# Performance work log

Measured on AMD Instinct MI355X. Metric: run time of the kernel, lower is better.

Reference implementation:

```python
import jax, jax.numpy as jnp
import numpy as np

LN_EPS = 1e-5


def _layer_norm(x, scale, bias):
    mu = jnp.mean(x, axis=-1, keepdims=True)
    var = jnp.mean(jnp.square(x - mu), axis=-1, keepdims=True)
    return (x - mu) * jax.lax.rsqrt(var + LN_EPS) * scale + bias


def setup_inputs() -> dict:
    key = jax.random.key(0)
    B, N, C_Z, C_H = 1, 512, 128, 128
    ks = jax.random.split(key, 8)
    s = 1.0 / np.sqrt(C_Z)
    inp = {
        "z": jax.random.normal(ks[0], (B, N, N, C_Z), dtype=jnp.float32),
        "mask": jnp.ones((B, N, N), dtype=jnp.float32),
        # gated / plain projections from c_z -> c_hidden
        "w_a_p": jax.random.normal(ks[1], (C_Z, C_H), dtype=jnp.float32) * s,
        "b_a_p": jnp.zeros((C_H,), dtype=jnp.float32),
        "w_a_g": jnp.zeros((C_Z, C_H), dtype=jnp.float32),  # gating init: zeros, bias ones
        "b_a_g": jnp.ones((C_H,), dtype=jnp.float32),
        "w_b_p": jax.random.normal(ks[2], (C_Z, C_H), dtype=jnp.float32) * s,
        "b_b_p": jnp.zeros((C_H,), dtype=jnp.float32),
        "w_b_g": jnp.zeros((C_Z, C_H), dtype=jnp.float32),
        "b_b_g": jnp.ones((C_H,), dtype=jnp.float32),
        # output gate c_z -> c_z (gating init)
        "w_g": jnp.zeros((C_Z, C_Z), dtype=jnp.float32),
        "b_g": jnp.ones((C_Z,), dtype=jnp.float32),
        # final projection c_hidden -> c_z ('final' init: zeros; use small randn for a nontrivial test)
        "w_z": jax.random.normal(ks[3], (C_H, C_Z), dtype=jnp.float32) * (1.0 / np.sqrt(C_H)),
        "b_z": jnp.zeros((C_Z,), dtype=jnp.float32),
        "ln_in_scale": jnp.ones((C_Z,), dtype=jnp.float32),
        "ln_in_bias": jnp.zeros((C_Z,), dtype=jnp.float32),
        "ln_out_scale": jnp.ones((C_H,), dtype=jnp.float32),
        "ln_out_bias": jnp.zeros((C_H,), dtype=jnp.float32),
    }
    return inp


def reference(z, mask, w_a_p, b_a_p, w_a_g, b_a_g, w_b_p, b_b_p, w_b_g, b_b_g,
              w_g, b_g, w_z, b_z, ln_in_scale, ln_in_bias, ln_out_scale, ln_out_bias):
    # tmu_type == 'outgoing'
    z = _layer_norm(z, ln_in_scale, ln_in_bias)          # [B,N,N,Cz]
    m = mask[..., None]                                   # [B,N,N,1]
    a = jax.nn.sigmoid(z @ w_a_g + b_a_g) * m * (z @ w_a_p + b_a_p)  # [B,N,N,Ch]
    b = jax.nn.sigmoid(z @ w_b_g + b_b_g) * m * (z @ w_b_p + b_b_p)  # [B,N,N,Ch]
    # outgoing: p[b,i,j,c] = sum_k a[b,i,k,c] * b[b,j,k,c]
    x = jnp.einsum("bikc,bjkc->bijc", a, b)              # [B,N,N,Ch]
    x = _layer_norm(x, ln_out_scale, ln_out_bias)
    x = x @ w_z + b_z                                    # [B,N,N,Cz]
    g = jax.nn.sigmoid(z @ w_g + b_g)                    # [B,N,N,Cz]
    return x * g
```

## Files before the change

kernel.cpp:

```cpp
#include <hip/hip_runtime.h>

typedef __attribute__((ext_vector_type(8))) short short8;
typedef __attribute__((ext_vector_type(4))) short short4v;
typedef __attribute__((ext_vector_type(4))) float float4v;

#define NDIM 512
#define NN (NDIM*NDIM)
#define CD 128

__device__ __forceinline__ unsigned short f2b(float f) {
  union { float f; unsigned u; } v; v.f = f;
  unsigned r = v.u + 0x7FFFu + ((v.u >> 16) & 1u);
  return (unsigned short)(r >> 16);
}
__device__ __forceinline__ float b2f(unsigned short h) {
  union { unsigned u; float f; } v; v.u = ((unsigned)h) << 16; return v.f;
}
__device__ __forceinline__ float sigmoidf_(float x) { return 1.f / (1.f + __expf(-x)); }
__device__ __forceinline__ unsigned pk2(float a, float b) {
  unsigned r;
  asm("v_cvt_pk_bf16_f32 %0, %1, %2" : "=v"(r) : "v"(a), "v"(b));
  return r;
}
__device__ __forceinline__ float4v mfma16(short8 a, short8 b, float4v c) {
  return __builtin_amdgcn_mfma_f32_16x16x32_bf16(a, b, c, 0, 0, 0);
}
__device__ __forceinline__ void gl_lds16(const short* g, short* l) {
  __builtin_amdgcn_global_load_lds(
      (const __attribute__((address_space(1))) unsigned int*)g,
      (__attribute__((address_space(3))) unsigned int*)l, 16, 0, 0);
}

__device__ __forceinline__ short8 fragr(const short* buf, int row, int j) {
  return *(const short8*)(buf + row * 128 + ((j ^ (row & 15)) << 3));
}
__device__ __forceinline__ void stg_w(short* buf, int row, int ku, unsigned v) {
  *(unsigned*)&buf[row * 128 + ((((ku >> 2) ^ (row & 15)) << 3) + ((ku & 3) << 1))] = v;
}

__global__ __launch_bounds__(256) void kPrepW(
    const float* __restrict__ w0, const float* __restrict__ w1,
    const float* __restrict__ w2, const float* __restrict__ w3,
    const float* __restrict__ w4, short* __restrict__ wt)
{
  const int wi = blockIdx.y;
  const float* W = wi==0 ? w0 : wi==1 ? w1 : wi==2 ? w2 : wi==3 ? w3 : w4;
  const int e = blockIdx.x * 256 + threadIdx.x;
  const int k = e >> 7, n = e & 127;
  wt[wi * 16384 + n * 128 + k] = (short)f2b(W[k * CD + n]);
}

__global__ __launch_bounds__(1024, 4) void kProj(
    const float* __restrict__ z, const float* __restrict__ mask,
    const short* __restrict__ wT,
    const float* __restrict__ b_a_p, const float* __restrict__ b_a_g,
    const float* __restrict__ b_b_p, const float* __restrict__ b_b_g,
    const float* __restrict__ b_g,
    const float* __restrict__ ln_s, const float* __restrict__ ln_b,
    short* __restrict__ a_t, short* __restrict__ b_t, short* __restrict__ g_out)
{
  __shared__ short zln[128 * 128];
  __shared__ short sS[128 * 128];
  __shared__ short wA[128 * 128];
  __shared__ short wB[128 * 128];
  const int t = threadIdx.x;
  const int r0 = blockIdx.x * 128;
  const int w = t >> 6, l = t & 63, lr = l & 15, lg = l >> 4;
  const int wr = (w >> 1) * 16;
  const int hc = (w & 1) * 64;

#define STAGE2(BUF, SLOT) do { _Pragma("unroll") for (int i_=0;i_<2;++i_) {  \
    int U_ = i_*1024 + t; int row_ = U_ >> 4, u_ = U_ & 15;                  \
    gl_lds16(wT + (SLOT)*16384 + row_*128 + ((u_^(row_&15))<<3), (BUF)+U_*8); } } while(0)

  STAGE2(wA, 1);
  STAGE2(wB, 0);

  {
    const int row = t >> 3, q = t & 7;
    const float* zp = z + (size_t)(r0 + row) * CD + q * 16;
    float x[16];
#pragma unroll
    for (int i = 0; i < 4; ++i) {
      float4v v = *(const float4v*)(zp + i * 4);
#pragma unroll
      for (int e = 0; e < 4; ++e) x[i*4+e] = v[e];
    }
    float s = 0.f;
#pragma unroll
    for (int i = 0; i < 16; ++i) s += x[i];
    s += __shfl_xor(s, 1, 64);
    s += __shfl_xor(s, 2, 64);
    s += __shfl_xor(s, 4, 64);
    const float mu = s * (1.f/128.f);
    float vs = 0.f;
#pragma unroll
    for (int i = 0; i < 16; ++i) { float d = x[i]-mu; vs += d*d; }
    vs += __shfl_xor(vs, 1, 64);
    vs += __shfl_xor(vs, 2, 64);
    vs += __shfl_xor(vs, 4, 64);
    const float rstd = rsqrtf(vs * (1.f/128.f) + 1e-5f);
#pragma unroll
    for (int i = 0; i < 16; i += 2) {
      int c = q*16 + i;
      float y0 = (x[i]  -mu)*rstd*ln_s[c]   + ln_b[c];
      float y1 = (x[i+1]-mu)*rstd*ln_s[c+1] + ln_b[c+1];
      int addr = row*128 + (((c>>3) ^ (row & 15)) << 3) + (c & 7);
      *(unsigned*)(&zln[addr]) = pk2(y0, y1);
    }
  }

  float bga[4], bpa[4], bgb[4], bpb[4];
#pragma unroll
  for (int cf = 0; cf < 4; ++cf) {
    int ci = hc + cf*16 + lr;
    bga[cf] = b_a_g[ci]; bpa[cf] = b_a_p[ci];
    bgb[cf] = b_b_g[ci]; bpb[cf] = b_b_p[ci];
  }
  float mrow[4];
#pragma unroll
  for (int jj = 0; jj < 4; ++jj) mrow[jj] = mask[r0 + wr + lg*4 + jj];

  __syncthreads();

  short8 af[4];
#pragma unroll
  for (int ks = 0; ks < 4; ++ks)
    af[ks] = fragr(zln, wr + lr, ks*4 + lg);

  float4v accG[4], accB[4];
  float sg[4][4];

#define ZERO4(A) do { _Pragma("unroll") for (int c_=0;c_<4;++c_) A[c_] = (float4v){0.f,0.f,0.f,0.f}; } while(0)

#define WP(ACC, BUF) do { ZERO4(ACC);                                      \
  _Pragma("unroll") for (int ks_=0; ks_<4; ++ks_)                          \
    _Pragma("unroll") for (int cf_=0; cf_<4; ++cf_) {                      \
      short8 wf_ = fragr(BUF, hc + cf_*16 + lr, ks_*4 + lg);               \
      ACC[cf_] = mfma16(af[ks_], wf_, ACC[cf_]);                           \
    } } while(0)

#define SIG4(BG) do { _Pragma("unroll") for (int cf_=0;cf_<4;++cf_)        \
    _Pragma("unroll") for (int j_=0;j_<4;++j_)                             \
      sg[cf_][j_] = sigmoidf_(accG[cf_][j_] + BG[cf_]) * mrow[j_]; } while(0)

#define PKAB(BP) do { _Pragma("unroll") for (int cf_=0;cf_<4;++cf_) {      \
    float v0_ = sg[cf_][0]*(accB[cf_][0]+BP[cf_]);                         \
    float v1_ = sg[cf_][1]*(accB[cf_][1]+BP[cf_]);                         \
    float v2_ = sg[cf_][2]*(accB[cf_][2]+BP[cf_]);                         \
    float v3_ = sg[cf_][3]*(accB[cf_][3]+BP[cf_]);                         \
    int ch_ = hc + cf_*16 + lr, ku_ = (wr >> 1) + lg*2;                    \
    stg_w(sS, ch_, ku_,   pk2(v0_, v1_));                                  \
    stg_w(sS, ch_, ku_+1, pk2(v2_, v3_)); } } while(0)

#define STORE64A(DST) do { int ch_ = t >> 3;                               \
  _Pragma("unroll") for (int i_=0;i_<2;++i_) {                             \
    int cL_ = (t & 7)*2 + i_;                                              \
    *(short8*)(DST + (size_t)ch_*NN + r0 + cL_*8) = fragr(sS, ch_, cL_);   \
  } } while(0)

  WP(accG, wA);
  WP(accB, wB);
  SIG4(bga);
  PKAB(bpa);
  __syncthreads();

  STAGE2(wA, 3);
  STAGE2(wB, 2);
  STORE64A(a_t);
  __syncthreads();

  WP(accG, wA);
  WP(accB, wB);
  SIG4(bgb);
  PKAB(bpb);
  __syncthreads();

  STAGE2(wA, 4);
  STORE64A(b_t);
  __syncthreads();

  {
    float4v accG2[4];
    ZERO4(accG2);
#pragma unroll
    for (int ks = 0; ks < 4; ++ks)
#pragma unroll
      for (int cf = 0; cf < 4; ++cf) {
        short8 wf = fragr(wA, hc + cf*16 + lr, ks*4 + lg);
        accG2[cf] = mfma16(wf, af[ks], accG2[cf]);
      }
#pragma unroll
    for (int cf = 0; cf < 4; ++cf) {
      float4v bgv = *(const float4v*)(b_g + hc + cf*16 + lg*4);
      float v0 = sigmoidf_(accG2[cf][0] + bgv[0]);
      float v1 = sigmoidf_(accG2[cf][1] + bgv[1]);
      float v2 = sigmoidf_(accG2[cf][2] + bgv[2]);
      float v3 = sigmoidf_(accG2[cf][3] + bgv[3]);
      int row = wr + lr, ku = (hc >> 1) + cf*8 + lg*2;
      stg_w(sS, row, ku,   pk2(v0, v1));
      stg_w(sS, row, ku+1, pk2(v2, v3));
    }
  }
  __syncthreads();

  {
    int row = t >> 3;
#pragma unroll
    for (int i = 0; i < 2; ++i) {
      int cL = (t & 7)*2 + i;
      *(short8*)(g_out + (size_t)(r0 + row)*CD + cL*8) = fragr(sS, row, cL);
    }
  }
}

__global__ __launch_bounds__(256, 2) void kEinsum(const short* __restrict__ a_t,
                                                  const short* __restrict__ b_t,
                                                  short* __restrict__ x_t)
{
  __shared__ short As[2][128 * 64];
  __shared__ short Bs[2][128 * 64];
  const int t = threadIdx.x;
  const int d = blockIdx.x;
  const int c = (d & 7) * 16 + (d >> 7);
  const int tile = (d >> 3) & 15;
  const int i0 = (tile >> 2) * 128;
  const int j0 = (tile & 3) * 128;
  const size_t abase = (size_t)c * NN;
  const int w = t >> 6, l = t & 63, lr = l & 15, lg = l >> 4;
  const int wr = w >> 1, wc = w & 1;

  const short* gA[4]; const short* gB[4]; int ldsU[4];
#pragma unroll
  for (int q = 0; q < 4; ++q) {
    int U = q * 256 + t;
    int row = U >> 3, u = U & 7;
    int swz = ((u ^ (row & 7)) << 3);
    gA[q] = a_t + abase + (size_t)(i0 + row) * NDIM + swz;
    gB[q] = b_t + abase + (size_t)(j0 + row) * NDIM + swz;
    ldsU[q] = U * 8;
  }

#define STAGE_E(buf, k0) do { _Pragma("unroll") for (int q_=0;q_<4;++q_) { \
    gl_lds16(gA[q_] + (k0), &As[buf][ldsU[q_]]);                           \
    gl_lds16(gB[q_] + (k0), &Bs[buf][ldsU[q_]]); } } while(0)

  float4v acc[4][4];
#pragma unroll
  for (int m = 0; m < 4; ++m)
#pragma unroll
    for (int n = 0; n < 4; ++n) acc[m][n] = (float4v){0.f,0.f,0.f,0.f};

  STAGE_E(0, 0);
  __syncthreads();
  int cur = 0;
#pragma unroll
  for (int it = 0; it < 8; ++it) {
    if (it < 7) STAGE_E(cur ^ 1, (it + 1) * 64);
    short8 afr[4][2], bfr[4][2];
#pragma unroll
    for (int m = 0; m < 4; ++m)
#pragma unroll
      for (int ks = 0; ks < 2; ++ks) {
        int row = wr*64 + m*16 + lr, j = ks*4 + lg;
        afr[m][ks] = *(const short8*)(&As[cur][row*64 + ((j ^ (row & 7)) << 3)]);
      }
#pragma unroll
    for (int n = 0; n < 4; ++n)
#pragma unroll
      for (int ks = 0; ks < 2; ++ks) {
        int row = wc*64 + n*16 + lr, j = ks*4 + lg;
        bfr[n][ks] = *(const short8*)(&Bs[cur][row*64 + ((j ^ (row & 7)) << 3)]);
      }
    __builtin_amdgcn_s_setprio(1);
#pragma unroll
    for (int ks = 0; ks < 2; ++ks)
#pragma unroll
      for (int m = 0; m < 4; ++m)
#pragma unroll
        for (int n = 0; n < 4; ++n)
          acc[m][n] = mfma16(bfr[n][ks], afr[m][ks], acc[m][n]);
    __builtin_amdgcn_s_setprio(0);
    __syncthreads();
    cur ^= 1;
  }
  short* Xs = &As[0][0];
#pragma unroll
  for (int m = 0; m < 4; ++m)
#pragma unroll
    for (int n = 0; n < 4; ++n) {
      int il = wr*64 + m*16 + lr;
      int ku = wc*32 + n*8 + lg*2;
      stg_w(Xs, il, ku,   pk2(acc[m][n][0], acc[m][n][1]));
      stg_w(Xs, il, ku+1, pk2(acc[m][n][2], acc[m][n][3]));
    }
  __syncthreads();
#pragma unroll
  for (int i = 0; i < 8; ++i) {
    int il = t >> 1, cL = (t & 1)*8 + i;
    *(short8*)(x_t + abase + (size_t)(i0 + il)*NDIM + j0 + cL*8) = fragr(Xs, il, cL);
  }
}

__global__ __launch_bounds__(256, 2) void kOut(
    const short* __restrict__ x_t, const short* __restrict__ g_in,
    const float* __restrict__ w_z, const float* __restrict__ b_z,
    const float* __restrict__ ln_s, const float* __restrict__ ln_b,
    float* __restrict__ out)
{
  __shared__ short xs[128 * 72];
  __shared__ short xln[64 * 128];
  __shared__ short sW[128 * 128];
  const int t = threadIdx.x;
  const int r0 = blockIdx.x * 64;
  const int w = t >> 6, l = t & 63, lr = l & 15, lg = l >> 4;

#pragma unroll
  for (int i = 0; i < 8; ++i) {
    int flat = i * 256 + t;
    int kp = flat >> 5, k = kp * 2, n4 = (flat & 31) * 4;
    float4v va = *(const float4v*)(w_z + (size_t)k * CD + n4);
    float4v vb = *(const float4v*)(w_z + (size_t)(k + 1) * CD + n4);
#pragma unroll
    for (int j = 0; j < 4; ++j) {
      int row = n4 + j;
      int addr = row * 128 + (((k >> 3) ^ (row & 15)) << 3) + (k & 7);
      *(unsigned*)(&sW[addr]) = pk2(va[j], vb[j]);
    }
  }
#pragma unroll
  for (int it = 0; it < 4; ++it) {
    int v = it * 256 + t; int cc = v >> 3; int u = v & 7;
    int up = u ^ ((cc >> 3) & 7);
    *(short8*)&xs[cc * 72 + up * 8] = *(const short8*)(x_t + (size_t)cc * NN + r0 + u * 8);
  }
  __syncthreads();
  {
    const int r = t >> 2, q = t & 3;
    float x[32];
#pragma unroll
    for (int i = 0; i < 32; ++i) {
      int c = q * 32 + i;
      x[i] = b2f((unsigned short)xs[c * 72 + (((r >> 3) ^ ((c >> 3) & 7)) << 3) + (r & 7)]);
    }
    float s = 0.f;
#pragma unroll
    for (int i = 0; i < 32; ++i) s += x[i];
    s += __shfl_xor(s, 1, 64);
    s += __shfl_xor(s, 2, 64);
    const float mu = s * (1.f/128.f);
    float vs = 0.f;
#pragma unroll
    for (int i = 0; i < 32; ++i) { float d = x[i]-mu; vs += d*d; }
    vs += __shfl_xor(vs, 1, 64);
    vs += __shfl_xor(vs, 2, 64);
    const float rstd = rsqrtf(vs * (1.f/128.f) + 1e-5f);
#pragma unroll
    for (int i = 0; i < 32; ++i) {
      int c = q*32 + i;
      float y = (x[i]-mu)*rstd*ln_s[c] + ln_b[c];
      xln[r*128 + (((c>>3) ^ (r & 15)) << 3) + (c & 7)] = (short)f2b(y);
    }
  }
  __syncthreads();
  short8 af[4];
#pragma unroll
  for (int ks = 0; ks < 4; ++ks)
    af[ks] = fragr(xln, w*16 + lr, ks*4 + lg);

  float4v acc[8];
#pragma unroll
  for (int cf = 0; cf < 8; ++cf) acc[cf] = (float4v){0.f,0.f,0.f,0.f};
#pragma unroll
  for (int ks = 0; ks < 4; ++ks)
#pragma unroll
    for (int cf = 0; cf < 8; ++cf) {
      short8 wf = fragr(sW, cf*16 + lr, ks*4 + lg);
      acc[cf] = mfma16(wf, af[ks], acc[cf]);
    }
  __syncthreads();
  float* fWs = (float*)sW;
  const int orow = r0 + w*16 + lr;
  const int rl = w*16 + lr;
#pragma unroll
  for (int cf = 0; cf < 8; ++cf) {
    float4v bzv = *(const float4v*)(b_z + cf*16 + lg*4);
    short4v gv = *(const short4v*)(g_in + (size_t)orow * CD + cf*16 + lg*4);
    float4v o;
#pragma unroll
    for (int j = 0; j < 4; ++j)
      o[j] = (acc[cf][j] + bzv[j]) * b2f((unsigned short)gv[j]);
    *(float4v*)&fWs[rl*128 + (((cf*4+lg) ^ (rl & 15)) << 2)] = o;
  }
  __syncthreads();
#pragma unroll
  for (int i = 0; i < 8; ++i) {
    int row = t >> 2, cL = (t & 3)*8 + i;
    *(float4v*)(out + (size_t)(r0 + row)*CD + cL*4) =
        *(const float4v*)&fWs[row*128 + ((cL ^ (row & 15)) << 2)];
  }
}

extern "C" void kernel_launch(void* const* d_in, const int* in_sizes, int n_in,
                              void* d_out, int out_size, void* d_ws, size_t ws_size,
                              hipStream_t stream) {
  (void)in_sizes; (void)n_in; (void)out_size; (void)ws_size;
  const float* z     = (const float*)d_in[0];
  const float* mask  = (const float*)d_in[1];
  const float* w_a_p = (const float*)d_in[2];
  const float* b_a_p = (const float*)d_in[3];
  const float* w_a_g = (const float*)d_in[4];
  const float* b_a_g = (const float*)d_in[5];
  const float* w_b_p = (const float*)d_in[6];
  const float* b_b_p = (const float*)d_in[7];
  const float* w_b_g = (const float*)d_in[8];
  const float* b_b_g = (const float*)d_in[9];
  const float* w_g   = (const float*)d_in[10];
  const float* b_g   = (const float*)d_in[11];
  const float* w_z   = (const float*)d_in[12];
  const float* b_z   = (const float*)d_in[13];
  const float* ln_i_s = (const float*)d_in[14];
  const float* ln_i_b = (const float*)d_in[15];
  const float* ln_o_s = (const float*)d_in[16];
  const float* ln_o_b = (const float*)d_in[17];

  short* a_t = (short*)d_ws;
  short* b_t = a_t + (size_t)CD*NN;
  short* g_s = b_t + (size_t)CD*NN;
  short* x_t = g_s + (size_t)CD*NN;
  short* wT  = x_t;

  hipLaunchKernelGGL(kPrepW, dim3(64, 5), dim3(256), 0, stream,
                     w_a_p, w_a_g, w_b_p, w_b_g, w_g, wT);
  hipLaunchKernelGGL(kProj, dim3(NN/128), dim3(1024), 0, stream,
                     z, mask, wT, b_a_p, b_a_g, b_b_p, b_b_g, b_g,
                     ln_i_s, ln_i_b, a_t, b_t, g_s);
  hipLaunchKernelGGL(kEinsum, dim3(2048), dim3(256), 0, stream, a_t, b_t, x_t);
  hipLaunchKernelGGL(kOut, dim3(NN/64), dim3(256), 0, stream,
                     x_t, g_s, w_z, b_z, ln_o_s, ln_o_b, (float*)d_out);
}
```

Baseline: 347.3 us.

## Restructure projection kernel to register-resident weights and pipelined 32-row tiles

The projection kernel moves from 1024-thread blocks that stage all weights into LDS to 256-thread blocks. Each block handles one half of the hidden channels for 128 rows and keeps its weight fragments in registers. It walks four 32-row sub-tiles with double-buffered LayerNorm output and prefetches the next sub-tile's z into registers, so global loads overlap with MFMA work. The aim is lower LDS use, higher occupancy and latency hiding, at the cost of recomputing LayerNorm twice (once per channel half) and higher register pressure from the 20 held weight fragments.

Result: slower. 359.9 us (+3.6%).

```diff
diff --git a/kernel.cpp b/kernel.cpp
--- a/kernel.cpp
+++ b/kernel.cpp
@@ -36,6 +36,18 @@
 }
 __device__ __forceinline__ void stg_w(short* buf, int row, int ku, unsigned v) {
   *(unsigned*)&buf[row * 128 + ((((ku >> 2) ^ (row & 15)) << 3) + ((ku & 3) << 1))] = v;
+}
+__device__ __forceinline__ short8 frag32(const short* buf, int ch, int j) {
+  return *(const short8*)(buf + ch * 32 + ((j ^ (ch & 3)) << 3));
+}
+__device__ __forceinline__ void stg32(short* buf, int ch, int ku, unsigned v) {
+  *(unsigned*)&buf[ch * 32 + ((((ku >> 2) ^ (ch & 3)) << 3) + ((ku & 3) << 1))] = v;
+}
+__device__ __forceinline__ short8 frag64(const short* buf, int row, int j) {
+  return *(const short8*)(buf + row * 64 + ((j ^ (row & 7)) << 3));
+}
+__device__ __forceinline__ void stg64(short* buf, int row, int ku, unsigned v) {
+  *(unsigned*)&buf[row * 64 + ((((ku >> 2) ^ (row & 7)) << 3) + ((ku & 3) << 1))] = v;
 }
 
 __global__ __launch_bounds__(256) void kPrepW(
@@ -50,7 +62,7 @@
   wt[wi * 16384 + n * 128 + k] = (short)f2b(W[k * CD + n]);
 }
 
-__global__ __launch_bounds__(1024, 4) void kProj(
+__global__ __launch_bounds__(256, 2) void kProj(
     const float* __restrict__ z, const float* __restrict__ mask,
     const short* __restrict__ wT,
     const float* __restrict__ b_a_p, const float* __restrict__ b_a_g,
@@ -59,159 +71,135 @@
     const float* __restrict__ ln_s, const float* __restrict__ ln_b,
     short* __restrict__ a_t, short* __restrict__ b_t, short* __restrict__ g_out)
 {
-  __shared__ short zln[128 * 128];
-  __shared__ short sS[128 * 128];
-  __shared__ short wA[128 * 128];
-  __shared__ short wB[128 * 128];
-  const int t = threadIdx.x;
-  const int r0 = blockIdx.x * 128;
-  const int w = t >> 6, l = t & 63, lr = l & 15, lg = l >> 4;
-  const int wr = (w >> 1) * 16;
-  const int hc = (w & 1) * 64;
-
-#define STAGE2(BUF, SLOT) do { _Pragma("unroll") for (int i_=0;i_<2;++i_) {  \
-    int U_ = i_*1024 + t; int row_ = U_ >> 4, u_ = U_ & 15;                  \
-    gl_lds16(wT + (SLOT)*16384 + row_*128 + ((u_^(row_&15))<<3), (BUF)+U_*8); } } while(0)
-
-  STAGE2(wA, 1);
-  STAGE2(wB, 0);
-
-  {
-    const int row = t >> 3, q = t & 7;
-    const float* zp = z + (size_t)(r0 + row) * CD + q * 16;
-    float x[16];
-#pragma unroll
-    for (int i = 0; i < 4; ++i) {
-      float4v v = *(const float4v*)(zp + i * 4);
-#pragma unroll
-      for (int e = 0; e < 4; ++e) x[i*4+e] = v[e];
-    }
-    float s = 0.f;
-#pragma unroll
-    for (int i = 0; i < 16; ++i) s += x[i];
-    s += __shfl_xor(s, 1, 64);
-    s += __shfl_xor(s, 2, 64);
-    s += __shfl_xor(s, 4, 64);
-    const float mu = s * (1.f/128.f);
-    float vs = 0.f;
-#pragma unroll
-    for (int i = 0; i < 16; ++i) { float d = x[i]-mu; vs += d*d; }
-    vs += __shfl_xor(vs, 1, 64);
-    vs += __shfl_xor(vs, 2, 64);
-    vs += __shfl_xor(vs, 4, 64);
-    const float rstd = rsqrtf(vs * (1.f/128.f) + 1e-5f);
-#pragma unroll
-    for (int i = 0; i < 16; i += 2) {
-      int c = q*16 + i;
-      float y0 = (x[i]  -mu)*rstd*ln_s[c]   + ln_b[c];
-      float y1 = (x[i+1]-mu)*rstd*ln_s[c+1] + ln_b[c+1];
-      int addr = row*128 + (((c>>3) ^ (row & 15)) << 3) + (c & 7);
-      *(unsigned*)(&zln[addr]) = pk2(y0, y1);
-    }
-  }
-
-  float bga[4], bpa[4], bgb[4], bpb[4];
-#pragma unroll
-  for (int cf = 0; cf < 4; ++cf) {
-    int ci = hc + cf*16 + lr;
-    bga[cf] = b_a_g[ci]; bpa[cf] = b_a_p[ci];
-    bgb[cf] = b_b_g[ci]; bpb[cf] = b_b_p[ci];
-  }
-  float mrow[4];
-#pragma unroll
-  for (int jj = 0; jj < 4; ++jj) mrow[jj] = mask[r0 + wr + lg*4 + jj];
-
-  __syncthreads();
-
-  short8 af[4];
-#pragma unroll
-  for (int ks = 0; ks < 4; ++ks)
-    af[ks] = fragr(zln, wr + lr, ks*4 + lg);
-
-  float4v accG[4], accB[4];
-  float sg[4][4];
-
-#define ZERO4(A) do { _Pragma("unroll") for (int c_=0;c_<4;++c_) A[c_] = (float4v){0.f,0.f,0.f,0.f}; } while(0)
-
-#define WP(ACC, BUF) do { ZERO4(ACC);                                      \
-  _Pragma("unroll") for (int ks_=0; ks_<4; ++ks_)                          \
-    _Pragma("unroll") for (int cf_=0; cf_<4; ++cf_) {                      \
-      short8 wf_ = fragr(BUF, hc + cf_*16 + lr, ks_*4 + lg);               \
-      ACC[cf_] = mfma16(af[ks_], wf_, ACC[cf_]);                           \
-    } } while(0)
-
-#define SIG4(BG) do { _Pragma("unroll") for (int cf_=0;cf_<4;++cf_)        \
-    _Pragma("unroll") for (int j_=0;j_<4;++j_)                             \
-      sg[cf_][j_] = sigmoidf_(accG[cf_][j_] + BG[cf_]) * mrow[j_]; } while(0)
-
-#define PKAB(BP) do { _Pragma("unroll") for (int cf_=0;cf_<4;++cf_) {      \
-    float v0_ = sg[cf_][0]*(accB[cf_][0]+BP[cf_]);                         \
-    float v1_ = sg[cf_][1]*(accB[cf_][1]+BP[cf_]);                         \
-    float v2_ = sg[cf_][2]*(accB[cf_][2]+BP[cf_]);                         \
-    float v3_ = sg[cf_][3]*(accB[cf_][3]+BP[cf_]);                         \
-    int ch_ = hc + cf_*16 + lr, ku_ = (wr >> 1) + lg*2;                    \
-    stg_w(sS, ch_, ku_,   pk2(v0_, v1_));                                  \
-    stg_w(sS, ch_, ku_+1, pk2(v2_, v3_)); } } while(0)
-
-#define STORE64A(DST) do { int ch_ = t >> 3;                               \
-  _Pragma("unroll") for (int i_=0;i_<2;++i_) {                             \
-    int cL_ = (t & 7)*2 + i_;                                              \
-    *(short8*)(DST + (size_t)ch_*NN + r0 + cL_*8) = fragr(sS, ch_, cL_);   \
-  } } while(0)
-
-  WP(accG, wA);
-  WP(accB, wB);
-  SIG4(bga);
-  PKAB(bpa);
-  __syncthreads();
-
-  STAGE2(wA, 3);
-  STAGE2(wB, 2);
-  STORE64A(a_t);
-  __syncthreads();
-
-  WP(accG, wA);
-  WP(accB, wB);
-  SIG4(bgb);
-  PKAB(bpb);
-  __syncthreads();
-
-  STAGE2(wA, 4);
-  STORE64A(b_t);
-  __syncthreads();
-
-  {
-    float4v accG2[4];
-    ZERO4(accG2);
+  __shared__ short zln[2][32 * 128];
+  __shared__ short sSa[64 * 32];
+  __shared__ short sSb[64 * 32];
+  __shared__ short sSg[32 * 64];
+
+  const int tid = threadIdx.x;
+  const int bid = blockIdx.x;
+  const int sw = (bid & 7) * 512 + (bid >> 3);
+  const int ch_half = sw & 1;
+  const int tg = sw >> 1;
+  const int r0 = tg * 128;
+  const int w = tid >> 6, l = tid & 63, lr = l & 15, lg = l >> 4;
+  const int chw = ch_half * 64 + w * 16;
+  const int lrow = tid >> 3, q = tid & 7;
+
+  short8 wfr[5][4];
+#pragma unroll
+  for (int s = 0; s < 5; ++s)
 #pragma unroll
     for (int ks = 0; ks < 4; ++ks)
-#pragma unroll
-      for (int cf = 0; cf < 4; ++cf) {
-        short8 wf = fragr(wA, hc + cf*16 + lr, ks*4 + lg);
-        accG2[cf] = mfma16(wf, af[ks], accG2[cf]);
-      }
-#pragma unroll
-    for (int cf = 0; cf < 4; ++cf) {
-      float4v bgv = *(const float4v*)(b_g + hc + cf*16 + lg*4);
-      float v0 = sigmoidf_(accG2[cf][0] + bgv[0]);
-      float v1 = sigmoidf_(accG2[cf][1] + bgv[1]);
-      float v2 = sigmoidf_(accG2[cf][2] + bgv[2]);
-      float v3 = sigmoidf_(accG2[cf][3] + bgv[3]);
-      int row = wr + lr, ku = (hc >> 1) + cf*8 + lg*2;
-      stg_w(sS, row, ku,   pk2(v0, v1));
-      stg_w(sS, row, ku+1, pk2(v2, v3));
-    }
-  }
-  __syncthreads();
-
-  {
-    int row = t >> 3;
-#pragma unroll
-    for (int i = 0; i < 2; ++i) {
-      int cL = (t & 7)*2 + i;
-      *(short8*)(g_out + (size_t)(r0 + row)*CD + cL*8) = fragr(sS, row, cL);
-    }
-  }
+      wfr[s][ks] = *(const short8*)(wT + s*16384 + (chw + lr)*128 + ks*32 + lg*8);
+
+  const float bga = b_a_g[chw + lr], bpa = b_a_p[chw + lr];
+  const float bgb = b_b_g[chw + lr], bpb = b_b_p[chw + lr];
+  const float4v bgv = *(const float4v*)(b_g + chw + lg*4);
+
+  const float* zbase = z + (size_t)(r0 + lrow) * CD + q * 16;
+  float4v zrA[4], zrB[4];
+#pragma unroll
+  for (int i = 0; i < 4; ++i) zrA[i] = *(const float4v*)(zbase + i * 4);
+
+#define WP2(ACC, WI) do {                                                   \
+  ACC[0] = (float4v){0.f,0.f,0.f,0.f}; ACC[1] = (float4v){0.f,0.f,0.f,0.f}; \
+  _Pragma("unroll") for (int ks_ = 0; ks_ < 4; ++ks_) {                     \
+    ACC[0] = mfma16(af[0][ks_], wfr[WI][ks_], ACC[0]);                      \
+    ACC[1] = mfma16(af[1][ks_], wfr[WI][ks_], ACC[1]); } } while(0)
+
+#define PROJ_TILE(T, ZR, ZN) do {                                           \
+  {                                       \
+    float s_ = 0.f;                                                         \
+    _Pragma("unroll") for (int i_ = 0; i_ < 4; ++i_)                        \
+      s_ += ZR[i_][0] + ZR[i_][1] + ZR[i_][2] + ZR[i_][3];                  \
+    s_ += __shfl_xor(s_, 1, 64); s_ += __shfl_xor(s_, 2, 64);               \
+    s_ += __shfl_xor(s_, 4, 64);                                            \
+    const float mu_ = s_ * (1.f/128.f);                                     \
+    float vs_ = 0.f;                                                        \
+    _Pragma("unroll") for (int i_ = 0; i_ < 16; ++i_) {                     \
+      float d_ = ZR[i_>>2][i_&3] - mu_; vs_ += d_*d_; }                     \
+    vs_ += __shfl_xor(vs_, 1, 64); vs_ += __shfl_xor(vs_, 2, 64);           \
+    vs_ += __shfl_xor(vs_, 4, 64);                                          \
+    const float rstd_ = rsqrtf(vs_ * (1.f/128.f) + 1e-5f);                  \
+    union { unsigned u4[4]; short8 s8; } lo_, hi_;                          \
+    _Pragma("unroll") for (int p_ = 0; p_ < 8; ++p_) {                      \
+      int c_ = q*16 + p_*2;                                                 \
+      float y0_ = (ZR[p_>>1][(p_&1)*2]   - mu_)*rstd_*ln_s[c_]   + ln_b[c_];     \
+      float y1_ = (ZR[p_>>1][(p_&1)*2+1] - mu_)*rstd_*ln_s[c_+1] + ln_b[c_+1];   \
+      if (p_ < 4) lo_.u4[p_] = pk2(y0_, y1_); else hi_.u4[p_-4] = pk2(y0_, y1_); \
+    }                                                                       \
+    short* zb_ = &zln[(T)&1][0];                                            \
+    *(short8*)&zb_[lrow*128 + (((q*2)   ^ (lrow&15))<<3)] = lo_.s8;         \
+    *(short8*)&zb_[lrow*128 + (((q*2+1) ^ (lrow&15))<<3)] = hi_.s8;         \
+  }                                                                         \
+  __syncthreads();        \
+  short8 af[2][4];                                                          \
+  _Pragma("unroll") for (int rg_ = 0; rg_ < 2; ++rg_)                       \
+    _Pragma("unroll") for (int ks_ = 0; ks_ < 4; ++ks_)                     \
+      af[rg_][ks_] = fragr(&zln[(T)&1][0], rg_*16 + lr, ks_*4 + lg);        \
+  float4v mr0 = *(const float4v*)(mask + r0 + (T)*32 + lg*4);               \
+  float4v mr1 = *(const float4v*)(mask + r0 + (T)*32 + 16 + lg*4);          \
+  if ((T) < 3) {             \
+    _Pragma("unroll") for (int i_ = 0; i_ < 4; ++i_)                        \
+      ZN[i_] = *(const float4v*)(zbase + ((T)+1)*32*CD + i_*4);             \
+  }                                                                         \
+  float4v aG[2], aB[2];                                                     \
+                                \
+  WP2(aG, 1); WP2(aB, 0);                                                   \
+  _Pragma("unroll") for (int rg_ = 0; rg_ < 2; ++rg_) {                     \
+    float4v mr_ = rg_ ? mr1 : mr0;                                          \
+    float s0_ = sigmoidf_(aG[rg_][0]+bga)*mr_[0];                           \
+    float s1_ = sigmoidf_(aG[rg_][1]+bga)*mr_[1];                           \
+    float s2_ = sigmoidf_(aG[rg_][2]+bga)*mr_[2];                           \
+    float s3_ = sigmoidf_(aG[rg_][3]+bga)*mr_[3];                           \
+    stg32(sSa, w*16+lr, rg_*8+lg*2,                                         \
+          pk2(s0_*(aB[rg_][0]+bpa), s1_*(aB[rg_][1]+bpa)));                 \
+    stg32(sSa, w*16+lr, rg_*8+lg*2+1,                                       \
+          pk2(s2_*(aB[rg_][2]+bpa), s3_*(aB[rg_][3]+bpa)));                 \
+  }                                                                         \
+                                \
+  WP2(aG, 3); WP2(aB, 2);                                                   \
+  _Pragma("unroll") for (int rg_ = 0; rg_ < 2; ++rg_) {                     \
+    float4v mr_ = rg_ ? mr1 : mr0;                                          \
+    float s0_ = sigmoidf_(aG[rg_][0]+bgb)*mr_[0];                           \
+    float s1_ = sigmoidf_(aG[rg_][1]+bgb)*mr_[1];                           \
+    float s2_ = sigmoidf_(aG[rg_][2]+bgb)*mr_[2];                           \
+    float s3_ = sigmoidf_(aG[rg_][3]+bgb)*mr_[3];                           \
+    stg32(sSb, w*16+lr, rg_*8+lg*2,                                         \
+          pk2(s0_*(aB[rg_][0]+bpb), s1_*(aB[rg_][1]+bpb)));                 \
+    stg32(sSb, w*16+lr, rg_*8+lg*2+1,                                       \
+          pk2(s2_*(aB[rg_][2]+bpb), s3_*(aB[rg_][3]+bpb)));                 \
+  }                                                                         \
+       \
+  _Pragma("unroll") for (int rg_ = 0; rg_ < 2; ++rg_)                       \
+    aG[rg_] = (float4v){0.f,0.f,0.f,0.f};                                   \
+  _Pragma("unroll") for (int ks_ = 0; ks_ < 4; ++ks_) {                     \
+    aG[0] = mfma16(wfr[4][ks_], af[0][ks_], aG[0]);                         \
+    aG[1] = mfma16(wfr[4][ks_], af[1][ks_], aG[1]);                         \
+  }                                                                         \
+  _Pragma("unroll") for (int rg_ = 0; rg_ < 2; ++rg_) {                     \
+    float g0_ = sigmoidf_(aG[rg_][0] + bgv[0]);                             \
+    float g1_ = sigmoidf_(aG[rg_][1] + bgv[1]);                             \
+    float g2_ = sigmoidf_(aG[rg_][2] + bgv[2]);                             \
+    float g3_ = sigmoidf_(aG[rg_][3] + bgv[3]);                             \
+    stg64(sSg, rg_*16+lr, w*8+lg*2,   pk2(g0_, g1_));                       \
+    stg64(sSg, rg_*16+lr, w*8+lg*2+1, pk2(g2_, g3_));                       \
+  }                                                                         \
+  __syncthreads();                                       \
+  { int chL_ = tid >> 2, jj_ = tid & 3;                                     \
+    size_t go_ = (size_t)(ch_half*64 + chL_)*NN + r0 + (T)*32 + jj_*8;      \
+    *(short8*)(a_t + go_) = frag32(sSa, chL_, jj_);                         \
+    *(short8*)(b_t + go_) = frag32(sSb, chL_, jj_); }                       \
+  { int rw_ = tid >> 3, jj_ = tid & 7;                                      \
+    *(short8*)(g_out + (size_t)(r0 + (T)*32 + rw_)*CD + ch_half*64 + jj_*8) \
+        = frag64(sSg, rw_, jj_); }                                          \
+} while(0)
+
+  PROJ_TILE(0, zrA, zrB);
+  PROJ_TILE(1, zrB, zrA);
+  PROJ_TILE(2, zrA, zrB);
+  PROJ_TILE(3, zrB, zrA);
 }
 
 __global__ __launch_bounds__(256, 2) void kEinsum(const short* __restrict__ a_t,
@@ -432,7 +420,7 @@
 
   hipLaunchKernelGGL(kPrepW, dim3(64, 5), dim3(256), 0, stream,
                      w_a_p, w_a_g, w_b_p, w_b_g, w_g, wT);
-  hipLaunchKernelGGL(kProj, dim3(NN/128), dim3(1024), 0, stream,
+  hipLaunchKernelGGL(kProj, dim3(4096), dim3(256), 0, stream,
                      z, mask, wT, b_a_p, b_a_g, b_b_p, b_b_g, b_g,
                      ln_i_s, ln_i_b, a_t, b_t, g_s);
   hipLaunchKernelGGL(kEinsum, dim3(2048), dim3(256), 0, stream, a_t, b_t, x_t);
```
